# Kernel optimization log

Measured on AMD Instinct MI355X. Metric: run time of the kernel, lower is better.

## Reference

```python
import jax, jax.numpy as jnp
import numpy as np

D_MODEL = 1024
NUM_HEADS = 16
HEAD_DIM = D_MODEL // NUM_HEADS


def setup_inputs() -> dict:
    key = jax.random.key(0)
    ks = jax.random.split(key, 5)
    B, S = 4, 2048
    x = jax.random.normal(ks[0], (B, S, D_MODEL), dtype=jnp.float32)
    scale = 1.0 / np.sqrt(D_MODEL)
    W_qkv = jax.random.normal(ks[1], (D_MODEL, 3 * D_MODEL), dtype=jnp.float32) * scale
    b_qkv = jnp.zeros((3 * D_MODEL,), dtype=jnp.float32)
    W_out = jax.random.normal(ks[2], (D_MODEL, D_MODEL), dtype=jnp.float32) * scale
    b_out = jnp.zeros((D_MODEL,), dtype=jnp.float32)
    return {"x": x, "W_qkv": W_qkv, "b_qkv": b_qkv, "W_out": W_out, "b_out": b_out}


def reference(x, W_qkv, b_qkv, W_out, b_out):
    B, S, D = x.shape
    H, hd = NUM_HEADS, HEAD_DIM
    qkv = x @ W_qkv + b_qkv                       # [B,S,3D]
    qkv = qkv.reshape(B, S, H, 3 * hd).transpose(0, 2, 1, 3)  # [B,H,S,3hd]
    q, k, v = jnp.split(qkv, 3, axis=-1)          # each [B,H,S,hd]
    scores = jnp.einsum('bhqd,bhkd->bhqk', q, k) / np.sqrt(hd)
    attn = jax.nn.softmax(scores, axis=-1)        # dropout: eval mode (identity)
    out = jnp.einsum('bhqk,bhkd->bhqd', attn, v)  # [B,H,S,hd]
    out = out.transpose(0, 2, 1, 3).reshape(B, S, D)
    return out @ W_out + b_out
```

## Files before the change

kernel.cpp:

```cpp
#include <hip/hip_runtime.h>
#include <cstdint>
#include <cstddef>

#define NUM_HEADS 16
#define HEAD_DIM  64
#define DMODEL    1024
#define BATCH     4
#define SEQ       2048
#define MROWS     (BATCH*SEQ)
#define N_QKV     (3*DMODEL)

#define QSCALE 0.18033688011111793f

typedef __attribute__((ext_vector_type(8))) short bf16x8;
typedef __attribute__((ext_vector_type(4))) float f32x4;
typedef __attribute__((ext_vector_type(16))) float f32x16;
typedef __attribute__((ext_vector_type(4))) uint32_t u32x4;

__device__ __forceinline__ short f2bf(float f){
  union { float f; uint32_t u; } w; w.f = f;
  uint32_t r = w.u + 0x7fffu + ((w.u >> 16) & 1u);
  return (short)(r >> 16);
}

typedef __attribute__((address_space(3))) short       lds_short_t;
typedef __attribute__((address_space(1))) const short glb_short_t;

__device__ __forceinline__ void gload_lds16(const short* g, short* lds){
  __builtin_amdgcn_global_load_lds((glb_short_t*)g, (lds_short_t*)lds, 16, 0, 0);
}

__device__ __forceinline__ void plane32_swap(uint32_t &a, uint32_t &b){
#if __has_builtin(__builtin_amdgcn_permlane32_swap)
  auto r = __builtin_amdgcn_permlane32_swap(a, b, false, false);
  a = r[0]; b = r[1];
#else
  asm volatile("v_permlane32_swap_b32 %0, %1" : "+v"(a), "+v"(b));
#endif
}

__device__ __forceinline__ float exp2r(float x){
#if __has_builtin(__builtin_amdgcn_exp2f)
  return __builtin_amdgcn_exp2f(x);
#else
  return exp2f(x);
#endif
}

__device__ __forceinline__ float max3f(float a, float b, float c){
  float d; asm("v_max3_f32 %0, %1, %2, %3" : "=v"(d) : "v"(a), "v"(b), "v"(c));
  return d;
}

__device__ __forceinline__ float max16(const f32x16& p){
  float a0 = max3f(p[0],  p[1],  p[2]);
  float a1 = max3f(p[3],  p[4],  p[5]);
  float a2 = max3f(p[6],  p[7],  p[8]);
  float a3 = max3f(p[9],  p[10], p[11]);
  float a4 = max3f(p[12], p[13], p[14]);
  return fmaxf(max3f(a0, a1, a2), max3f(a3, a4, p[15]));
}

__global__ void k_cvt(const float* __restrict__ in, short* __restrict__ out, int n4){
  int i = blockIdx.x*256 + threadIdx.x;
  if (i >= n4) return;
  float4 v = reinterpret_cast<const float4*>(in)[i];
  short4 o; o.x = f2bf(v.x); o.y = f2bf(v.y); o.z = f2bf(v.z); o.w = f2bf(v.w);
  reinterpret_cast<short4*>(out)[i] = o;
}

__global__ void k_cvt_t(const float* __restrict__ in, short* __restrict__ out, int R, int C){
  __shared__ short t[64][65];
  int cb = blockIdx.x*64, rb = blockIdx.y*64;
  int tx = threadIdx.x & 63, ty = threadIdx.x >> 6;
  #pragma unroll
  for (int i = ty; i < 64; i += 4)
    t[i][tx] = f2bf(in[(size_t)(rb+i)*C + cb + tx]);
  __syncthreads();
  #pragma unroll
  for (int i = ty; i < 64; i += 4)
    out[(size_t)(cb+i)*R + rb + tx] = t[tx][i];
}

template<int MODE>
__global__ __launch_bounds__(256, 3) void k_gemm(
    const short* __restrict__ A, const short* __restrict__ Bt,
    const float* __restrict__ bias,
    short* __restrict__ Qb, short* __restrict__ Kb, short* __restrict__ Vt,
    float* __restrict__ Out, int K)
{
  __shared__ short As[2][128*32];
  __shared__ short Bs[2][128*32];
  const int lane = threadIdx.x & 63, wave = threadIdx.x >> 6;
  const int wr = wave >> 1, wc = wave & 1;
  const int m0 = blockIdx.y * 128, n0 = blockIdx.x * 128;

  f32x4 acc[4][4] = {};

  const int srow = lane >> 2;
  const int sseg = (lane & 3) ^ (srow & 3);
  const int nkt = K >> 5;

  auto stage = [&](int bsel, int kt){
    #pragma unroll
    for (int c = 0; c < 2; ++c){
      const int ch = wave*2 + c;
      const int r  = ch*16 + srow;
      gload_lds16(A  + (size_t)(m0 + r)*K + kt*32 + sseg*8, &As[bsel][ch*512]);
      gload_lds16(Bt + (size_t)(n0 + r)*K + kt*32 + sseg*8, &Bs[bsel][ch*512]);
    }
  };

  stage(0, 0);
  __syncthreads();

  for (int kt = 0; kt < nkt; ++kt){
    const int cur = kt & 1;
    if (kt + 1 < nkt) stage(cur ^ 1, kt + 1);

    bf16x8 af[4], bfr[4];
    #pragma unroll
    for (int m = 0; m < 4; ++m){
      const int ra = wr*64 + m*16 + (lane & 15);
      af[m]  = *reinterpret_cast<const bf16x8*>(&As[cur][ra*32 + (((lane>>4) ^ (ra & 3))*8)]);
      const int rb = wc*64 + m*16 + (lane & 15);
      bfr[m] = *reinterpret_cast<const bf16x8*>(&Bs[cur][rb*32 + (((lane>>4) ^ (rb & 3))*8)]);
    }
    #pragma unroll
    for (int m = 0; m < 4; ++m)
      #pragma unroll
      for (int n = 0; n < 4; ++n)
        acc[m][n] = __builtin_amdgcn_mfma_f32_16x16x32_bf16(af[m], bfr[n], acc[m][n], 0, 0, 0);

    __syncthreads();
  }

  #pragma unroll
  for (int m = 0; m < 4; ++m){
    const int row = m0 + wr*64 + m*16 + ((lane>>4)<<2);
    #pragma unroll
    for (int n = 0; n < 4; ++n){
      const int col = n0 + wc*64 + n*16 + (lane & 15);
      const float bv = bias[col];
      #pragma unroll
      for (int i = 0; i < 4; ++i){
        const int r = row + i;
        const float v = acc[m][n][i] + bv;
        if (MODE == 0){
          const int h = col / 192, q = col % 192;
          const int b = r >> 11, s = r & 2047;
          const int bh = b*NUM_HEADS + h;
          if (q < 64)       Qb[((size_t)bh*SEQ + s)*64 + q]          = f2bf(v * QSCALE);
          else if (q < 128) Kb[((size_t)bh*SEQ + s)*64 + (q-64)]     = f2bf(v);
          else              Vt[((size_t)bh*64 + (q-128))*SEQ + s]    = f2bf(v);
        } else {
          Out[(size_t)r*DMODEL + col] = v;
        }
      }
    }
  }
}

__global__ __launch_bounds__(256, 3) void k_attn(
    const short* __restrict__ Qb, const short* __restrict__ Kb,
    const short* __restrict__ Vt, short* __restrict__ Ob)
{
  __shared__ short Ks[2][64*64];
  __shared__ short Vs[2][64*64];
  const int lane = threadIdx.x & 63, wave = threadIdx.x >> 6;
  const int l31 = lane & 31, hi = lane >> 5;
  const int bh = blockIdx.y;
  const int q0 = blockIdx.x*128 + wave*32;

  bf16x8 qf[4];
  {
    const short* qrow = Qb + ((size_t)bh*SEQ + q0 + l31)*64;
    #pragma unroll
    for (int ks = 0; ks < 4; ++ks)
      qf[ks] = *reinterpret_cast<const bf16x8*>(qrow + ks*16 + hi*8);
  }

  f32x16 oacc[2] = {};
  float mrun = -1e30f, lrun = 0.f;

  const int r8 = lane >> 3, sg = lane & 7;

  auto stage = [&](int bsel, int kt){
    #pragma unroll
    for (int c = 0; c < 2; ++c){
      const int ch  = wave*2 + c;
      const int row = ch*8 + r8;
      const int seg = sg ^ (row & 7);
      gload_lds16(Kb + ((size_t)bh*SEQ + kt*64 + row)*64 + seg*8, &Ks[bsel][ch*512]);
      gload_lds16(Vt + ((size_t)bh*64 + row)*SEQ + kt*64 + seg*8, &Vs[bsel][ch*512]);
    }
  };

  stage(0, 0);
  __syncthreads();

  for (int kt = 0; kt < SEQ/64; ++kt){
    const int cur = kt & 1;
    if (kt < SEQ/64 - 1) stage(cur ^ 1, kt + 1);

    f32x16 p[2] = {};
    #pragma unroll
    for (int t = 0; t < 2; ++t){
      const int key = t*32 + l31;
      const short* krow = &Ks[cur][key*64];
      const int sw = key & 7;
      #pragma unroll
      for (int ks = 0; ks < 4; ++ks){
        const bf16x8 kf = *reinterpret_cast<const bf16x8*>(krow + (((2*ks + hi) ^ sw) * 8));
        p[t] = __builtin_amdgcn_mfma_f32_32x32x16_bf16(kf, qf[ks], p[t], 0, 0, 0);
      }
    }

    float pmax = fmaxf(max16(p[0]), max16(p[1]));
    pmax = fmaxf(pmax, __shfl_xor(pmax, 32));

    if (__any(pmax - mrun > 8.f)){
      const float mnew = fmaxf(mrun, pmax);
      const float corr = exp2r(mrun - mnew);
      lrun *= corr;
      mrun = mnew;
      #pragma unroll
      for (int r = 0; r < 16; ++r){
        const int qr = (r & 3) + 8*(r >> 2) + 4*hi;
        const float cf = __shfl(corr, qr);
        oacc[0][r] *= cf;
        oacc[1][r] *= cf;
      }
    }

    float ps = 0.f;
    #pragma unroll
    for (int t = 0; t < 2; ++t)
      #pragma unroll
      for (int r = 0; r < 16; ++r){
        const float e = exp2r(p[t][r] - mrun);
        p[t][r] = e;
        ps += e;
      }
    ps += __shfl_xor(ps, 32);
    lrun += ps;

    uint32_t pk[2][2][4];
    #pragma unroll
    for (int t = 0; t < 2; ++t)
      #pragma unroll
      for (int c = 0; c < 2; ++c)
        #pragma unroll
        for (int w = 0; w < 4; ++w){
          uint32_t rr;
          asm("v_cvt_pk_bf16_f32 %0, %1, %2"
              : "=v"(rr) : "v"(p[t][8*c + 2*w]), "v"(p[t][8*c + 2*w + 1]));
          pk[t][c][w] = rr;
        }

    #pragma unroll
    for (int ks = 0; ks < 4; ++ks){
      const int t = ks >> 1, c = ks & 1;
      uint32_t w0 = pk[t][c][0], w2 = pk[t][c][2];
      uint32_t w1 = pk[t][c][1], w3 = pk[t][c][3];
      plane32_swap(w0, w2);
      plane32_swap(w1, w3);
      u32x4 fwv; fwv[0] = w0; fwv[1] = w1; fwv[2] = w2; fwv[3] = w3;
      const bf16x8 pa = __builtin_bit_cast(bf16x8, fwv);
      #pragma unroll
      for (int dt = 0; dt < 2; ++dt){
        const int d = dt*32 + l31;
        const bf16x8 vf = *reinterpret_cast<const bf16x8*>(
            &Vs[cur][d*64 + (((2*ks + hi) ^ (d & 7)) * 8)]);
        oacc[dt] = __builtin_amdgcn_mfma_f32_32x32x16_bf16(pa, vf, oacc[dt], 0, 0, 0);
      }
    }
    __syncthreads();
  }

  const float linv = 1.f / lrun;
  const int b = bh >> 4, h = bh & 15;
  #pragma unroll
  for (int r = 0; r < 16; ++r){
    const int qr = (r & 3) + 8*(r >> 2) + 4*hi;
    const float li = __shfl(linv, qr);
    const int s = q0 + qr;
    #pragma unroll
    for (int dt = 0; dt < 2; ++dt){
      const int d = dt*32 + l31;
      Ob[((size_t)b*SEQ + s)*DMODEL + h*64 + d] = f2bf(oacc[dt][r] * li);
    }
  }
}

extern "C" void kernel_launch(void* const* d_in, const int* in_sizes, int n_in,
                              void* d_out, int out_size, void* d_ws, size_t ws_size,
                              hipStream_t stream)
{
  const float* x    = (const float*)d_in[0];
  const float* Wqkv = (const float*)d_in[1];
  const float* bqkv = (const float*)d_in[2];
  const float* Wout = (const float*)d_in[3];
  const float* bout = (const float*)d_in[4];
  float* out = (float*)d_out;

  short* ws  = (short*)d_ws;
  short* xb  = ws;
  short* wqt = xb  + (size_t)MROWS*DMODEL;
  short* wot = wqt + (size_t)N_QKV*DMODEL;
  short* Qb  = wot + (size_t)DMODEL*DMODEL;
  short* Kb  = Qb  + (size_t)MROWS*DMODEL;
  short* Vt  = Kb  + (size_t)MROWS*DMODEL;

  k_cvt<<<dim3(MROWS*DMODEL/4/256), dim3(256), 0, stream>>>(x, xb, MROWS*DMODEL/4);
  k_cvt_t<<<dim3(N_QKV/64, DMODEL/64), dim3(256), 0, stream>>>(Wqkv, wqt, DMODEL, N_QKV);
  k_cvt_t<<<dim3(DMODEL/64, DMODEL/64), dim3(256), 0, stream>>>(Wout, wot, DMODEL, DMODEL);

  k_gemm<0><<<dim3(N_QKV/128, MROWS/128), dim3(256), 0, stream>>>(
      xb, wqt, bqkv, Qb, Kb, Vt, nullptr, DMODEL);

  k_attn<<<dim3(SEQ/128, BATCH*NUM_HEADS), dim3(256), 0, stream>>>(Qb, Kb, Vt, xb);

  k_gemm<1><<<dim3(DMODEL/128, MROWS/128), dim3(256), 0, stream>>>(
      xb, wot, bout, nullptr, nullptr, nullptr, out, DMODEL);
}
```

Measured before the change: 293.6 us.

## Use 256x256x64 tiled GEMM with 512 threads for QKV projection

Adds a dedicated QKV-projection GEMM kernel with a 256x256 output tile, a K-step of 64 and 8 waves, each computing a 128x64 sub-tile with XOR-swizzled LDS. The larger tile raises arithmetic intensity and cuts the global/LDS load traffic per MFMA compared with the old 128x128x32 kernel. The out-projection keeps the old 128-tile kernel, now specialised to fp32 output. In exchange, LDS use grows to 128KB per block and register pressure rises. The grid shrinks to 384 blocks, which may hurt occupancy and wave balance across CUs.

```diff
diff --git a/kernel.cpp b/kernel.cpp
--- a/kernel.cpp
+++ b/kernel.cpp
@@ -82,12 +82,90 @@
     out[(size_t)(cb+i)*R + rb + tx] = t[tx][i];
 }
 
-template<int MODE>
-__global__ __launch_bounds__(256, 3) void k_gemm(
+__global__ __launch_bounds__(512, 2) void k_gemm256(
     const short* __restrict__ A, const short* __restrict__ Bt,
     const float* __restrict__ bias,
     short* __restrict__ Qb, short* __restrict__ Kb, short* __restrict__ Vt,
-    float* __restrict__ Out, int K)
+    int K)
+{
+  __shared__ short As[2][256*64];
+  __shared__ short Bs[2][256*64];
+  const int lane = threadIdx.x & 63, wave = threadIdx.x >> 6;
+  const int wr = wave >> 2, wc = wave & 3;
+  const int m0 = blockIdx.y * 256, n0 = blockIdx.x * 256;
+
+  f32x4 acc[8][4] = {};
+
+  const int nkt = K >> 6;
+
+  auto stage = [&](int bsel, int t){
+    #pragma unroll
+    for (int c = 0; c < 4; ++c){
+      const int ch   = (wave*4 + c)*64 + lane;
+      const int row  = ch >> 3;
+      const int ss   = (ch & 7) ^ (row & 7);
+      gload_lds16(A  + (size_t)(m0 + row)*K + t*64 + ss*8, &As[bsel][(wave*4 + c)*512]);
+      gload_lds16(Bt + (size_t)(n0 + row)*K + t*64 + ss*8, &Bs[bsel][(wave*4 + c)*512]);
+    }
+  };
+
+  stage(0, 0);
+  __syncthreads();
+
+  for (int t = 0; t < nkt; ++t){
+    const int cur = t & 1;
+    if (t + 1 < nkt) stage(cur ^ 1, t + 1);
+
+    bf16x8 bfr[4][2];
+    #pragma unroll
+    for (int ni = 0; ni < 4; ++ni){
+      const int rb = wc*64 + ni*16 + (lane & 15);
+      #pragma unroll
+      for (int ks = 0; ks < 2; ++ks)
+        bfr[ni][ks] = *reinterpret_cast<const bf16x8*>(
+            &Bs[cur][rb*64 + (((ks*4 + (lane>>4)) ^ (rb & 7))*8)]);
+    }
+    #pragma unroll
+    for (int mi = 0; mi < 8; ++mi){
+      const int ra = wr*128 + mi*16 + (lane & 15);
+      bf16x8 af0 = *reinterpret_cast<const bf16x8*>(
+          &As[cur][ra*64 + ((((lane>>4)    ) ^ (ra & 7))*8)]);
+      bf16x8 af1 = *reinterpret_cast<const bf16x8*>(
+          &As[cur][ra*64 + (((4 + (lane>>4)) ^ (ra & 7))*8)]);
+      #pragma unroll
+      for (int ni = 0; ni < 4; ++ni){
+        acc[mi][ni] = __builtin_amdgcn_mfma_f32_16x16x32_bf16(af0, bfr[ni][0], acc[mi][ni], 0, 0, 0);
+        acc[mi][ni] = __builtin_amdgcn_mfma_f32_16x16x32_bf16(af1, bfr[ni][1], acc[mi][ni], 0, 0, 0);
+      }
+    }
+    __syncthreads();
+  }
+
+  #pragma unroll
+  for (int mi = 0; mi < 8; ++mi){
+    const int row = m0 + wr*128 + mi*16 + ((lane>>4)<<2);
+    #pragma unroll
+    for (int ni = 0; ni < 4; ++ni){
+      const int col = n0 + wc*64 + ni*16 + (lane & 15);
+      const float bv = bias[col];
+      const int h = col / 192, q = col % 192;
+      #pragma unroll
+      for (int i = 0; i < 4; ++i){
+        const int r = row + i;
+        const float v = acc[mi][ni][i] + bv;
+        const int b = r >> 11, s = r & 2047;
+        const int bh = b*NUM_HEADS + h;
+        if (q < 64)       Qb[((size_t)bh*SEQ + s)*64 + q]          = f2bf(v * QSCALE);
+        else if (q < 128) Kb[((size_t)bh*SEQ + s)*64 + (q-64)]     = f2bf(v);
+        else              Vt[((size_t)bh*64 + (q-128))*SEQ + s]    = f2bf(v);
+      }
+    }
+  }
+}
+
+__global__ __launch_bounds__(256, 3) void k_gemm128(
+    const short* __restrict__ A, const short* __restrict__ Bt,
+    const float* __restrict__ bias, float* __restrict__ Out, int K)
 {
   __shared__ short As[2][128*32];
   __shared__ short Bs[2][128*32];
@@ -143,20 +221,8 @@
       const int col = n0 + wc*64 + n*16 + (lane & 15);
       const float bv = bias[col];
       #pragma unroll
-      for (int i = 0; i < 4; ++i){
-        const int r = row + i;
-        const float v = acc[m][n][i] + bv;
-        if (MODE == 0){
-          const int h = col / 192, q = col % 192;
-          const int b = r >> 11, s = r & 2047;
-          const int bh = b*NUM_HEADS + h;
-          if (q < 64)       Qb[((size_t)bh*SEQ + s)*64 + q]          = f2bf(v * QSCALE);
-          else if (q < 128) Kb[((size_t)bh*SEQ + s)*64 + (q-64)]     = f2bf(v);
-          else              Vt[((size_t)bh*64 + (q-128))*SEQ + s]    = f2bf(v);
-        } else {
-          Out[(size_t)r*DMODEL + col] = v;
-        }
-      }
+      for (int i = 0; i < 4; ++i)
+        Out[(size_t)(row + i)*DMODEL + col] = acc[m][n][i] + bv;
     }
   }
 }
@@ -316,11 +382,11 @@
   k_cvt_t<<<dim3(N_QKV/64, DMODEL/64), dim3(256), 0, stream>>>(Wqkv, wqt, DMODEL, N_QKV);
   k_cvt_t<<<dim3(DMODEL/64, DMODEL/64), dim3(256), 0, stream>>>(Wout, wot, DMODEL, DMODEL);
 
-  k_gemm<0><<<dim3(N_QKV/128, MROWS/128), dim3(256), 0, stream>>>(
-      xb, wqt, bqkv, Qb, Kb, Vt, nullptr, DMODEL);
+  k_gemm256<<<dim3(N_QKV/256, MROWS/256), dim3(512), 0, stream>>>(
+      xb, wqt, bqkv, Qb, Kb, Vt, DMODEL);
 
   k_attn<<<dim3(SEQ/128, BATCH*NUM_HEADS), dim3(256), 0, stream>>>(Qb, Kb, Vt, xb);
 
-  k_gemm<1><<<dim3(DMODEL/128, MROWS/128), dim3(256), 0, stream>>>(
-      xb, wot, bout, nullptr, nullptr, nullptr, out, DMODEL);
-}
+  k_gemm128<<<dim3(DMODEL/128, MROWS/128), dim3(256), 0, stream>>>(
+      xb, wot, bout, out, DMODEL);
+}
```

Result: slower. 304.4 us (+3.7%).

## Use 256x128 tiles with 512 threads for QKV GEMM; raise MFMA priority in attention

Applied to the files above, without the earlier changes.

Splits the templated GEMM into a dedicated QKV projection kernel with 256-row tiles and 8 waves sharing one B tile, and a plain 128x128 kernel for the output projection. The larger tile raises B-tile reuse and halves the number of blocks for the QKV GEMM, at the cost of more LDS and registers per block. The attention kernel also wraps its two MFMA phases in s_setprio so waves issuing matrix work are favoured over those doing softmax or loads. Occupancy changes and the altered wave scheduling could offset the gains.

```diff
diff --git a/kernel.cpp b/kernel.cpp
--- a/kernel.cpp
+++ b/kernel.cpp
@@ -82,12 +82,85 @@
     out[(size_t)(cb+i)*R + rb + tx] = t[tx][i];
 }
 
-template<int MODE>
-__global__ __launch_bounds__(256, 3) void k_gemm(
+__global__ __launch_bounds__(512, 4) void k_gemmA(
     const short* __restrict__ A, const short* __restrict__ Bt,
     const float* __restrict__ bias,
     short* __restrict__ Qb, short* __restrict__ Kb, short* __restrict__ Vt,
-    float* __restrict__ Out, int K)
+    int K)
+{
+  __shared__ short As[2][256*32];
+  __shared__ short Bs[2][128*32];
+  const int lane = threadIdx.x & 63, wave = threadIdx.x >> 6;
+  const int wr = wave >> 1, wc = wave & 1;
+  const int m0 = blockIdx.y * 256, n0 = blockIdx.x * 128;
+
+  f32x4 acc[4][4] = {};
+
+  const int nkt = K >> 5;
+
+  auto stage = [&](int bsel, int kt){
+    #pragma unroll
+    for (int c = 0; c < 2; ++c){
+      const int ch  = (wave*2 + c)*64 + lane;
+      const int row = ch >> 2;
+      const int ss  = (ch & 3) ^ (row & 3);
+      gload_lds16(A + (size_t)(m0 + row)*K + kt*32 + ss*8, &As[bsel][(wave*2 + c)*512]);
+    }
+    const int chB  = wave*64 + lane;
+    const int rowB = chB >> 2;
+    const int ssB  = (chB & 3) ^ (rowB & 3);
+    gload_lds16(Bt + (size_t)(n0 + rowB)*K + kt*32 + ssB*8, &Bs[bsel][wave*512]);
+  };
+
+  stage(0, 0);
+  __syncthreads();
+
+  for (int kt = 0; kt < nkt; ++kt){
+    const int cur = kt & 1;
+    if (kt + 1 < nkt) stage(cur ^ 1, kt + 1);
+
+    bf16x8 af[4], bfr[4];
+    #pragma unroll
+    for (int m = 0; m < 4; ++m){
+      const int ra = wr*64 + m*16 + (lane & 15);
+      af[m]  = *reinterpret_cast<const bf16x8*>(&As[cur][ra*32 + (((lane>>4) ^ (ra & 3))*8)]);
+      const int rb = wc*64 + m*16 + (lane & 15);
+      bfr[m] = *reinterpret_cast<const bf16x8*>(&Bs[cur][rb*32 + (((lane>>4) ^ (rb & 3))*8)]);
+    }
+    #pragma unroll
+    for (int m = 0; m < 4; ++m)
+      #pragma unroll
+      for (int n = 0; n < 4; ++n)
+        acc[m][n] = __builtin_amdgcn_mfma_f32_16x16x32_bf16(af[m], bfr[n], acc[m][n], 0, 0, 0);
+
+    __syncthreads();
+  }
+
+  #pragma unroll
+  for (int m = 0; m < 4; ++m){
+    const int row = m0 + wr*64 + m*16 + ((lane>>4)<<2);
+    #pragma unroll
+    for (int n = 0; n < 4; ++n){
+      const int col = n0 + wc*64 + n*16 + (lane & 15);
+      const float bv = bias[col];
+      const int h = col / 192, q = col % 192;
+      #pragma unroll
+      for (int i = 0; i < 4; ++i){
+        const int r = row + i;
+        const float v = acc[m][n][i] + bv;
+        const int b = r >> 11, s = r & 2047;
+        const int bh = b*NUM_HEADS + h;
+        if (q < 64)       Qb[((size_t)bh*SEQ + s)*64 + q]          = f2bf(v * QSCALE);
+        else if (q < 128) Kb[((size_t)bh*SEQ + s)*64 + (q-64)]     = f2bf(v);
+        else              Vt[((size_t)bh*64 + (q-128))*SEQ + s]    = f2bf(v);
+      }
+    }
+  }
+}
+
+__global__ __launch_bounds__(256, 3) void k_gemm128(
+    const short* __restrict__ A, const short* __restrict__ Bt,
+    const float* __restrict__ bias, float* __restrict__ Out, int K)
 {
   __shared__ short As[2][128*32];
   __shared__ short Bs[2][128*32];
@@ -143,20 +216,8 @@
       const int col = n0 + wc*64 + n*16 + (lane & 15);
       const float bv = bias[col];
       #pragma unroll
-      for (int i = 0; i < 4; ++i){
-        const int r = row + i;
-        const float v = acc[m][n][i] + bv;
-        if (MODE == 0){
-          const int h = col / 192, q = col % 192;
-          const int b = r >> 11, s = r & 2047;
-          const int bh = b*NUM_HEADS + h;
-          if (q < 64)       Qb[((size_t)bh*SEQ + s)*64 + q]          = f2bf(v * QSCALE);
-          else if (q < 128) Kb[((size_t)bh*SEQ + s)*64 + (q-64)]     = f2bf(v);
-          else              Vt[((size_t)bh*64 + (q-128))*SEQ + s]    = f2bf(v);
-        } else {
-          Out[(size_t)r*DMODEL + col] = v;
-        }
-      }
+      for (int i = 0; i < 4; ++i)
+        Out[(size_t)(row + i)*DMODEL + col] = acc[m][n][i] + bv;
     }
   }
 }
@@ -204,6 +265,7 @@
     if (kt < SEQ/64 - 1) stage(cur ^ 1, kt + 1);
 
     f32x16 p[2] = {};
+    __builtin_amdgcn_s_setprio(1);
     #pragma unroll
     for (int t = 0; t < 2; ++t){
       const int key = t*32 + l31;
@@ -215,6 +277,7 @@
         p[t] = __builtin_amdgcn_mfma_f32_32x32x16_bf16(kf, qf[ks], p[t], 0, 0, 0);
       }
     }
+    __builtin_amdgcn_s_setprio(0);
 
     float pmax = fmaxf(max16(p[0]), max16(p[1]));
     pmax = fmaxf(pmax, __shfl_xor(pmax, 32));
@@ -258,6 +321,7 @@
           pk[t][c][w] = rr;
         }
 
+    __builtin_amdgcn_s_setprio(1);
     #pragma unroll
     for (int ks = 0; ks < 4; ++ks){
       const int t = ks >> 1, c = ks & 1;
@@ -275,6 +339,7 @@
         oacc[dt] = __builtin_amdgcn_mfma_f32_32x32x16_bf16(pa, vf, oacc[dt], 0, 0, 0);
       }
     }
+    __builtin_amdgcn_s_setprio(0);
     __syncthreads();
   }
 
@@ -316,11 +381,11 @@
   k_cvt_t<<<dim3(N_QKV/64, DMODEL/64), dim3(256), 0, stream>>>(Wqkv, wqt, DMODEL, N_QKV);
   k_cvt_t<<<dim3(DMODEL/64, DMODEL/64), dim3(256), 0, stream>>>(Wout, wot, DMODEL, DMODEL);
 
-  k_gemm<0><<<dim3(N_QKV/128, MROWS/128), dim3(256), 0, stream>>>(
-      xb, wqt, bqkv, Qb, Kb, Vt, nullptr, DMODEL);
+  k_gemmA<<<dim3(N_QKV/128, MROWS/256), dim3(512), 0, stream>>>(
+      xb, wqt, bqkv, Qb, Kb, Vt, DMODEL);
 
   k_attn<<<dim3(SEQ/128, BATCH*NUM_HEADS), dim3(256), 0, stream>>>(Qb, Kb, Vt, xb);
 
-  k_gemm<1><<<dim3(DMODEL/128, MROWS/128), dim3(256), 0, stream>>>(
-      xb, wot, bout, nullptr, nullptr, nullptr, out, DMODEL);
-}
+  k_gemm128<<<dim3(DMODEL/128, MROWS/128), dim3(256), 0, stream>>>(
+      xb, wot, bout, out, DMODEL);
+}
```

Measured after the change: 303.3 us. 1.03x slower.
